# Optimization experiments

Hardware: AMD Instinct MI355X
Metric: run time of the kernel (lower is better)

## Reference

```python
import jax, jax.numpy as jnp
import numpy as np

BATCH = 8192
IN_FEATURES = 1024
OUT_FEATURES = 1024
GRID_SIZE = 5
SPLINE_ORDER = 3
GRID_MIN, GRID_MAX = -1.0, 1.0
NUM_BASES = GRID_SIZE + SPLINE_ORDER  # 8
GRID_LEN = GRID_SIZE + 2 * SPLINE_ORDER + 1  # 12


def setup_inputs() -> dict:
    key = jax.random.key(0)
    k1, k2, k3 = jax.random.split(key, 3)
    x = jax.random.normal(k1, (BATCH, IN_FEATURES), dtype=jnp.float32)
    base_weight = jax.random.normal(k2, (OUT_FEATURES, IN_FEATURES), dtype=jnp.float32) * 0.1
    spline_weight = jax.random.normal(k3, (OUT_FEATURES, IN_FEATURES, NUM_BASES), dtype=jnp.float32) * 0.1
    grid = jnp.linspace(GRID_MIN, GRID_MAX, GRID_LEN, dtype=jnp.float32)  # buffer, not learned
    return {"x": x, "base_weight": base_weight, "spline_weight": spline_weight, "grid": grid}


def _bspline_basis(xc, grid, order):
    """Iterative Cox-de Boor DP, vectorized over all features and basis indices.
    xc: [B, F] clamped inputs; grid: [G] uniform knots (all denominators > 0).
    Returns [B, F, G - order - 1] = [B, F, NUM_BASES]."""
    G = grid.shape[0]
    xe = xc[..., None]  # [B, F, 1]
    # k = 0: indicator of knot interval, matches (x >= grid[i]) & (x < grid[i+1])
    B = ((xe >= grid[:-1]) & (xe < grid[1:])).astype(xc.dtype)  # [B, F, G-1]
    for k in range(1, order + 1):
        left = (xe - grid[: G - k - 1]) / (grid[k : G - 1] - grid[: G - k - 1]) * B[..., :-1]
        right = (grid[k + 1 : G] - xe) / (grid[k + 1 : G] - grid[1 : G - k]) * B[..., 1:]
        B = left + right  # [B, F, G-1-k]
    return B


def reference(x, base_weight, spline_weight, grid):
    # base path: SiLU activation then linear
    base_output = jax.nn.silu(x) @ base_weight.T  # [B, out]
    # spline path: B-spline basis per feature, weighted sum over (in, basis)
    x_clamped = jnp.clip(x, GRID_MIN * 0.99, GRID_MAX * 0.99)
    basis = _bspline_basis(x_clamped, grid, SPLINE_ORDER)  # [B, in, NUM_BASES]
    spline_output = jnp.einsum("bin,oin->bo", basis, spline_weight)
    return base_output + spline_output
```

## Files before the change

### kernel.cpp

```cpp
#include <hip/hip_runtime.h>
#include <stdint.h>

typedef _Float16 f16;
typedef __attribute__((ext_vector_type(8))) _Float16 f16x8;
typedef __attribute__((ext_vector_type(4))) float f32x4;

#define BATCH 8192
#define INF   1024
#define OUTF  1024
#define KTOT  9216
#define NT    72
#define CONV_BLOCKS 4608

__device__ __forceinline__ void gload16(const void* g, void* l) {
  __builtin_amdgcn_global_load_lds(
      (const __attribute__((address_space(1))) uint32_t*)g,
      (__attribute__((address_space(3))) uint32_t*)l, 16, 0, 0);
}

__global__ __launch_bounds__(256) void fused_prep_kernel(
    const float* __restrict__ bw, const float* __restrict__ sw,
    const float* __restrict__ x, const float* __restrict__ grid,
    f16* __restrict__ Wb, f16* __restrict__ Abuf)
{
  int blk = blockIdx.x;
  if (blk < CONV_BLOCKS) {
    int idx = blk * 256 + threadIdx.x;
    int o = idx / 1152;
    int r = idx - o * 1152;
    int k8 = r * 8;
    const float* src = (k8 < INF) ? (bw + (size_t)o * INF + k8)
                                  : (sw + (size_t)o * (INF * 8) + (k8 - INF));
    float4 v0 = *(const float4*)src;
    float4 v1 = *(const float4*)(src + 4);
    f16x8 ov;
    ov[0] = (f16)v0.x; ov[1] = (f16)v0.y; ov[2] = (f16)v0.z; ov[3] = (f16)v0.w;
    ov[4] = (f16)v1.x; ov[5] = (f16)v1.y; ov[6] = (f16)v1.z; ov[7] = (f16)v1.w;
    *(f16x8*)(Wb + (size_t)o * KTOT + k8) = ov;
    return;
  }

  int q = (blk - CONV_BLOCKS) * 256 + threadIdx.x;
  int b = q >> 8;
  int i0 = (q & 255) << 2;
  float4 xv = *(const float4*)(x + ((size_t)b << 10) + i0);
  float xa[4] = {xv.x, xv.y, xv.z, xv.w};

  float g[12];
#pragma unroll
  for (int j = 0; j < 12; ++j) g[j] = grid[j];
  float H  = g[1] - g[0];
  float r1 = 1.0f / H;
  float r2 = 0.5f * r1;
  float r3 = (1.0f / 3.0f) * r1;

  f16 sil[4];
  f16x8 bas[4];
#pragma unroll
  for (int e = 0; e < 4; ++e) {
    float v = xa[e];
    sil[e] = (f16)(v / (1.0f + __expf(-v)));
    float xe = fminf(fmaxf(v, -0.99f), 0.99f);
    float Bv[11];
#pragma unroll
    for (int j = 0; j < 11; ++j) Bv[j] = (xe >= g[j] && xe < g[j + 1]) ? 1.0f : 0.0f;
#pragma unroll
    for (int j = 0; j < 10; ++j) Bv[j] = (xe - g[j]) * r1 * Bv[j] + (g[j + 2] - xe) * r1 * Bv[j + 1];
#pragma unroll
    for (int j = 0; j < 9; ++j)  Bv[j] = (xe - g[j]) * r2 * Bv[j] + (g[j + 3] - xe) * r2 * Bv[j + 1];
#pragma unroll
    for (int j = 0; j < 8; ++j)  Bv[j] = (xe - g[j]) * r3 * Bv[j] + (g[j + 4] - xe) * r3 * Bv[j + 1];
#pragma unroll
    for (int n = 0; n < 8; ++n) bas[e][n] = (f16)Bv[n];
  }
  f16* row = Abuf + (size_t)b * KTOT;
  *(uint64_t*)(row + i0) = *(const uint64_t*)sil;
  f16* bp = row + INF + (size_t)i0 * 8;
#pragma unroll
  for (int e = 0; e < 4; ++e) *(f16x8*)(bp + e * 8) = bas[e];
}

#define LDA(base, m, s) (*(const f16x8*)((base) + ((wr*128 + (m)*16 + la) * 64 + ((((s)*4 + lb) ^ lasw) * 8))))
#define LDB(base, n, s) (*(const f16x8*)((base) + ((wcn*64 + (n)*16 + la) * 64 + ((((s)*4 + lb) ^ lasw) * 8))))

#define MFMA1(m, n, s) acc[m][n] = __builtin_amdgcn_mfma_f32_16x16x32_f16(af[m][s], bf[n][s], acc[m][n], 0, 0, 0)
#define MFMA_S0(m0) do { \
  MFMA1(m0,0,0);   MFMA1(m0,1,0);   MFMA1(m0,2,0);   MFMA1(m0,3,0); \
  MFMA1(m0+1,0,0); MFMA1(m0+1,1,0); MFMA1(m0+1,2,0); MFMA1(m0+1,3,0); } while (0)
#define MFMA_S1(m0) do { \
  MFMA1(m0,0,1);   MFMA1(m0,1,1);   MFMA1(m0,2,1);   MFMA1(m0,3,1); \
  MFMA1(m0+1,0,1); MFMA1(m0+1,1,1); MFMA1(m0+1,2,1); MFMA1(m0+1,3,1); } while (0)

#define SCHED0 __builtin_amdgcn_sched_barrier(0)
#define SBARF do { __builtin_amdgcn_s_barrier(); SCHED0; } while (0)

template <bool ATOMIC>
__global__ __launch_bounds__(512, 2) void kan_gemm_kernel(
    const f16* __restrict__ A, const f16* __restrict__ W,
    float* __restrict__ C, float* __restrict__ P1)
{
  __shared__ __align__(16) f16 lsA[2 * 256 * 64];
  __shared__ __align__(16) f16 lsB[2 * 256 * 64];

  const size_t K = KTOT;
  int bid = blockIdx.x;
  int xcd = bid & 7;
  int u   = bid >> 3;
  int tm  = xcd * 4 + (u & 3);
  int tn  = (u >> 2) & 3;
  int split = u >> 4;
  size_t kbase = (size_t)split * (NT * 64);

  int tid = threadIdx.x;
  int w = tid >> 6, l = tid & 63;
  int wr = w >> 2, wcn = w & 3;
  int la = l & 15, lb = l >> 4, lasw = la & 7;

  int rh = tid >> 3;
  int sc = (tid & 7) ^ (rh & 7);
  const f16* aSrc0 = A + (size_t)(tm * 256 + rh) * K + kbase + sc * 8;
  const f16* bSrc0 = W + (size_t)(tn * 256 + rh) * K + kbase + sc * 8;

  auto stage = [&](int h) {
    if (h >= 4 * NT) return;
    int tile = h >> 2, ty = h & 3, half = ty & 1;
    size_t koff = (size_t)tile * 64;
    if (ty < 2) {
      const f16* s = aSrc0 + (size_t)half * 128 * K + koff;
      f16* d = lsA + (tile & 1) * 16384 + half * 8192 + w * 512;
      gload16(s, d);
      gload16(s + 64 * K, d + 4096);
    } else {
      const f16* s = bSrc0 + (size_t)half * 128 * K + koff;
      f16* d = lsB + (tile & 1) * 16384 + half * 8192 + w * 512;
      gload16(s, d);
      gload16(s + 64 * K, d + 4096);
    }
  };

  f16x8 af[8][2], bf[4][2];
  f32x4 acc[8][4] = {};

  stage(0); stage(1); stage(2); stage(3);
  asm volatile("s_waitcnt vmcnt(0)" ::: "memory");
  SCHED0;

  for (int t = 0; t < NT; ++t) {
    const f16* bA = lsA + (t & 1) * 16384;
    const f16* bB = lsB + (t & 1) * 16384;
    int h1 = 4 * (t + 1);

    SBARF;
    stage(h1 + 0); stage(h1 + 1);
    stage(h1 + 2); stage(h1 + 3);
    __builtin_amdgcn_s_setprio(1);
    af[0][0] = LDA(bA, 0, 0); af[1][0] = LDA(bA, 1, 0);
    bf[0][0] = LDB(bB, 0, 0); bf[1][0] = LDB(bB, 1, 0);
    bf[2][0] = LDB(bB, 2, 0); bf[3][0] = LDB(bB, 3, 0);
    af[0][1] = LDA(bA, 0, 1); af[1][1] = LDA(bA, 1, 1);
    bf[0][1] = LDB(bB, 0, 1); bf[1][1] = LDB(bB, 1, 1);
    bf[2][1] = LDB(bB, 2, 1); bf[3][1] = LDB(bB, 3, 1);
    af[2][0] = LDA(bA, 2, 0); af[3][0] = LDA(bA, 3, 0);
    MFMA_S0(0);
    af[2][1] = LDA(bA, 2, 1); af[3][1] = LDA(bA, 3, 1);
    MFMA_S1(0);
    af[4][0] = LDA(bA, 4, 0); af[5][0] = LDA(bA, 5, 0);
    MFMA_S0(2);
    af[4][1] = LDA(bA, 4, 1); af[5][1] = LDA(bA, 5, 1);
    MFMA_S1(2);
    af[6][0] = LDA(bA, 6, 0); af[7][0] = LDA(bA, 7, 0);
    MFMA_S0(4);
    af[6][1] = LDA(bA, 6, 1); af[7][1] = LDA(bA, 7, 1);
    MFMA_S1(4);
    MFMA_S0(6);
    MFMA_S1(6);
    __builtin_amdgcn_s_setprio(0);
    asm volatile("s_waitcnt vmcnt(0)" ::: "memory");
    SCHED0;
  }

  int rowBase = tm * 256 + wr * 128 + lb * 4;
  int colBase = tn * 256 + wcn * 64 + la;
  float* dst = ATOMIC ? C : (split ? P1 : C);
#pragma unroll
  for (int m = 0; m < 8; ++m)
#pragma unroll
    for (int n = 0; n < 4; ++n) {
      int col = colBase + n * 16;
#pragma unroll
      for (int j = 0; j < 4; ++j) {
        int row = rowBase + m * 16 + j;
        if (ATOMIC) atomicAdd(&C[(size_t)row * OUTF + col], acc[m][n][j]);
        else        dst[(size_t)row * OUTF + col] = acc[m][n][j];
      }
    }
}

__global__ __launch_bounds__(256) void reduce_kernel(
    float* __restrict__ out, const float* __restrict__ p)
{
  size_t i = ((size_t)blockIdx.x * 256 + threadIdx.x) * 4;
  f32x4 a = *(f32x4*)(out + i);
  f32x4 b = *(const f32x4*)(p + i);
  a += b;
  *(f32x4*)(out + i) = a;
}

extern "C" void kernel_launch(void* const* d_in, const int* in_sizes, int n_in,
                              void* d_out, int out_size, void* d_ws, size_t ws_size,
                              hipStream_t stream)
{
  const float* x  = (const float*)d_in[0];
  const float* bw = (const float*)d_in[1];
  const float* sw = (const float*)d_in[2];
  const float* gr = (const float*)d_in[3];
  float* out = (float*)d_out;

  f16* Wb = (f16*)d_ws;
  size_t wBytes = (size_t)OUTF * KTOT * sizeof(f16);
  f16* Abuf = (f16*)((char*)d_ws + wBytes);
  size_t aBytes = (size_t)BATCH * KTOT * sizeof(f16);
  size_t oBytes = (size_t)BATCH * OUTF * sizeof(float);

  int prepBlocks = (BATCH * INF / 4) / 256;
  fused_prep_kernel<<<CONV_BLOCKS + prepBlocks, 256, 0, stream>>>(
      bw, sw, x, gr, Wb, Abuf);

  if (ws_size >= wBytes + aBytes + oBytes) {
    float* P1 = (float*)((char*)d_ws + wBytes + aBytes);
    kan_gemm_kernel<false><<<256, 512, 0, stream>>>(Abuf, Wb, out, P1);
    reduce_kernel<<<(int)(oBytes / sizeof(float) / 4 / 256), 256, 0, stream>>>(out, P1);
  } else {
    hipMemsetAsync(d_out, 0, oBytes, stream);
    kan_gemm_kernel<true><<<256, 512, 0, stream>>>(Abuf, Wb, out, nullptr);
  }
}
```

Measured before the change: 227.9 us.

## Split GEMM main loop into barrier-synchronized load/MFMA phases

Restructures each K-iteration of the fp16 MFMA GEMM into four phases. In each phase the waves load a pair of A fragments from LDS (plus B fragments in the first phase) and issue part of the next tile's global-to-LDS copies. They then meet at a workgroup barrier, wait on lgkmcnt, and run that phase's MFMAs at raised priority. The goal is to keep waves in lockstep, ping-pong style, so LDS reads and MFMA bursts from different waves or blocks interleave better. The cost is many more s_barriers per iteration and full LDS waits before each MFMA group, which can serialize work that was overlapped before.

After: 229.0 us. Within noise of the previous version (+0.5%).

```diff
diff --git a/kernel.cpp b/kernel.cpp
--- a/kernel.cpp
+++ b/kernel.cpp
@@ -92,7 +92,8 @@
   MFMA1(m0+1,0,1); MFMA1(m0+1,1,1); MFMA1(m0+1,2,1); MFMA1(m0+1,3,1); } while (0)
 
 #define SCHED0 __builtin_amdgcn_sched_barrier(0)
-#define SBARF do { __builtin_amdgcn_s_barrier(); SCHED0; } while (0)
+#define SBARF do { SCHED0; __builtin_amdgcn_s_barrier(); SCHED0; } while (0)
+#define LGKM0 do { asm volatile("s_waitcnt lgkmcnt(0)" ::: "memory"); SCHED0; } while (0)
 
 template <bool ATOMIC>
 __global__ __launch_bounds__(512, 2) void kan_gemm_kernel(
@@ -143,40 +144,51 @@
 
   stage(0); stage(1); stage(2); stage(3);
   asm volatile("s_waitcnt vmcnt(0)" ::: "memory");
-  SCHED0;
+  SBARF;
 
   for (int t = 0; t < NT; ++t) {
     const f16* bA = lsA + (t & 1) * 16384;
     const f16* bB = lsB + (t & 1) * 16384;
     int h1 = 4 * (t + 1);
 
-    SBARF;
-    stage(h1 + 0); stage(h1 + 1);
-    stage(h1 + 2); stage(h1 + 3);
-    __builtin_amdgcn_s_setprio(1);
-    af[0][0] = LDA(bA, 0, 0); af[1][0] = LDA(bA, 1, 0);
     bf[0][0] = LDB(bB, 0, 0); bf[1][0] = LDB(bB, 1, 0);
     bf[2][0] = LDB(bB, 2, 0); bf[3][0] = LDB(bB, 3, 0);
-    af[0][1] = LDA(bA, 0, 1); af[1][1] = LDA(bA, 1, 1);
     bf[0][1] = LDB(bB, 0, 1); bf[1][1] = LDB(bB, 1, 1);
     bf[2][1] = LDB(bB, 2, 1); bf[3][1] = LDB(bB, 3, 1);
-    af[2][0] = LDA(bA, 2, 0); af[3][0] = LDA(bA, 3, 0);
-    MFMA_S0(0);
-    af[2][1] = LDA(bA, 2, 1); af[3][1] = LDA(bA, 3, 1);
-    MFMA_S1(0);
-    af[4][0] = LDA(bA, 4, 0); af[5][0] = LDA(bA, 5, 0);
-    MFMA_S0(2);
-    af[4][1] = LDA(bA, 4, 1); af[5][1] = LDA(bA, 5, 1);
-    MFMA_S1(2);
-    af[6][0] = LDA(bA, 6, 0); af[7][0] = LDA(bA, 7, 0);
-    MFMA_S0(4);
-    af[6][1] = LDA(bA, 6, 1); af[7][1] = LDA(bA, 7, 1);
-    MFMA_S1(4);
-    MFMA_S0(6);
-    MFMA_S1(6);
+    af[0][0] = LDA(bA, 0, 0); af[0][1] = LDA(bA, 0, 1);
+    af[1][0] = LDA(bA, 1, 0); af[1][1] = LDA(bA, 1, 1);
+    stage(h1 + 0); stage(h1 + 1);
+    SBARF; LGKM0;
+    __builtin_amdgcn_s_setprio(1);
+    MFMA_S0(0); MFMA_S1(0);
+    __builtin_amdgcn_s_setprio(0);
+    SBARF;
+
+    af[2][0] = LDA(bA, 2, 0); af[2][1] = LDA(bA, 2, 1);
+    af[3][0] = LDA(bA, 3, 0); af[3][1] = LDA(bA, 3, 1);
+    stage(h1 + 2); stage(h1 + 3);
+    SBARF; LGKM0;
+    __builtin_amdgcn_s_setprio(1);
+    MFMA_S0(2); MFMA_S1(2);
+    __builtin_amdgcn_s_setprio(0);
+    SBARF;
+
+    af[4][0] = LDA(bA, 4, 0); af[4][1] = LDA(bA, 4, 1);
+    af[5][0] = LDA(bA, 5, 0); af[5][1] = LDA(bA, 5, 1);
+    SBARF; LGKM0;
+    __builtin_amdgcn_s_setprio(1);
+    MFMA_S0(4); MFMA_S1(4);
+    __builtin_amdgcn_s_setprio(0);
+    SBARF;
+
+    af[6][0] = LDA(bA, 6, 0); af[6][1] = LDA(bA, 6, 1);
+    af[7][0] = LDA(bA, 7, 0); af[7][1] = LDA(bA, 7, 1);
+    SBARF; LGKM0;
+    __builtin_amdgcn_s_setprio(1);
+    MFMA_S0(6); MFMA_S1(6);
     __builtin_amdgcn_s_setprio(0);
     asm volatile("s_waitcnt vmcnt(0)" ::: "memory");
-    SCHED0;
+    SBARF;
   }
 
   int rowBase = tm * 256 + wr * 128 + lb * 4;
```

## Shrink GEMM block to 128x256 tile with single-buffered LDS and mid-loop prefetch

Applied to the files above, without the earlier changes.

Each GEMM block changes from 512 threads with a 256x256 tile and double-buffered LDS to 256 threads with a 128x256 tile and single-buffered LDS. Grid size doubles to 512 blocks. The next tile's global-to-LDS loads are issued halfway through the MFMA work, after all LDS fragments have been read, so they overlap the remaining MFMAs. This lowers LDS use per block so more blocks can be resident, but it reduces reuse of the B tile and adds a second barrier per k-step.

After: 205.6 us. 9.8% less time.

```diff
diff --git a/kernel.cpp b/kernel.cpp
--- a/kernel.cpp
+++ b/kernel.cpp
@@ -80,7 +80,7 @@
   for (int e = 0; e < 4; ++e) *(f16x8*)(bp + e * 8) = bas[e];
 }
 
-#define LDA(base, m, s) (*(const f16x8*)((base) + ((wr*128 + (m)*16 + la) * 64 + ((((s)*4 + lb) ^ lasw) * 8))))
+#define LDA(base, m, s) (*(const f16x8*)((base) + (((m)*16 + la) * 64 + ((((s)*4 + lb) ^ lasw) * 8))))
 #define LDB(base, n, s) (*(const f16x8*)((base) + ((wcn*64 + (n)*16 + la) * 64 + ((((s)*4 + lb) ^ lasw) * 8))))
 
 #define MFMA1(m, n, s) acc[m][n] = __builtin_amdgcn_mfma_f32_16x16x32_f16(af[m][s], bf[n][s], acc[m][n], 0, 0, 0)
@@ -92,94 +92,88 @@
   MFMA1(m0+1,0,1); MFMA1(m0+1,1,1); MFMA1(m0+1,2,1); MFMA1(m0+1,3,1); } while (0)
 
 #define SCHED0 __builtin_amdgcn_sched_barrier(0)
-#define SBARF do { __builtin_amdgcn_s_barrier(); SCHED0; } while (0)
+#define SBARF  do { SCHED0; __builtin_amdgcn_s_barrier(); SCHED0; } while (0)
+#define LGKM0  do { asm volatile("s_waitcnt lgkmcnt(0)" ::: "memory"); SCHED0; } while (0)
 
 template <bool ATOMIC>
-__global__ __launch_bounds__(512, 2) void kan_gemm_kernel(
+__global__ __launch_bounds__(256, 2) void kan_gemm_kernel(
     const f16* __restrict__ A, const f16* __restrict__ W,
     float* __restrict__ C, float* __restrict__ P1)
 {
-  __shared__ __align__(16) f16 lsA[2 * 256 * 64];
-  __shared__ __align__(16) f16 lsB[2 * 256 * 64];
+  __shared__ __align__(16) f16 lsA[128 * 64];
+  __shared__ __align__(16) f16 lsB[256 * 64];
 
   const size_t K = KTOT;
   int bid = blockIdx.x;
   int xcd = bid & 7;
   int u   = bid >> 3;
-  int tm  = xcd * 4 + (u & 3);
-  int tn  = (u >> 2) & 3;
-  int split = u >> 4;
+  int tm  = xcd * 8 + (u & 7);
+  int tn  = (u >> 3) & 3;
+  int split = u >> 5;
   size_t kbase = (size_t)split * (NT * 64);
 
   int tid = threadIdx.x;
   int w = tid >> 6, l = tid & 63;
-  int wr = w >> 2, wcn = w & 3;
+  int wcn = w;
   int la = l & 15, lb = l >> 4, lasw = la & 7;
 
   int rh = tid >> 3;
   int sc = (tid & 7) ^ (rh & 7);
-  const f16* aSrc0 = A + (size_t)(tm * 256 + rh) * K + kbase + sc * 8;
+  const f16* aSrc0 = A + (size_t)(tm * 128 + rh) * K + kbase + sc * 8;
   const f16* bSrc0 = W + (size_t)(tn * 256 + rh) * K + kbase + sc * 8;
 
-  auto stage = [&](int h) {
-    if (h >= 4 * NT) return;
-    int tile = h >> 2, ty = h & 3, half = ty & 1;
-    size_t koff = (size_t)tile * 64;
-    if (ty < 2) {
-      const f16* s = aSrc0 + (size_t)half * 128 * K + koff;
-      f16* d = lsA + (tile & 1) * 16384 + half * 8192 + w * 512;
-      gload16(s, d);
-      gload16(s + 64 * K, d + 4096);
-    } else {
-      const f16* s = bSrc0 + (size_t)half * 128 * K + koff;
-      f16* d = lsB + (tile & 1) * 16384 + half * 8192 + w * 512;
-      gload16(s, d);
-      gload16(s + 64 * K, d + 4096);
-    }
+  auto stageA = [&](int t) {
+    size_t koff = (size_t)t * 64;
+#pragma unroll
+    for (int ln = 0; ln < 4; ++ln)
+      gload16(aSrc0 + (size_t)ln * 32 * K + koff, lsA + ln * 2048 + w * 512);
+  };
+  auto stageB = [&](int t) {
+    size_t koff = (size_t)t * 64;
+#pragma unroll
+    for (int ln = 0; ln < 8; ++ln)
+      gload16(bSrc0 + (size_t)ln * 32 * K + koff, lsB + ln * 2048 + w * 512);
   };
 
   f16x8 af[8][2], bf[4][2];
   f32x4 acc[8][4] = {};
 
-  stage(0); stage(1); stage(2); stage(3);
-  asm volatile("s_waitcnt vmcnt(0)" ::: "memory");
-  SCHED0;
+  stageA(0); stageB(0);
 
   for (int t = 0; t < NT; ++t) {
-    const f16* bA = lsA + (t & 1) * 16384;
-    const f16* bB = lsB + (t & 1) * 16384;
-    int h1 = 4 * (t + 1);
-
+    asm volatile("s_waitcnt vmcnt(0)" ::: "memory");
     SBARF;
-    stage(h1 + 0); stage(h1 + 1);
-    stage(h1 + 2); stage(h1 + 3);
+
+    bf[0][0] = LDB(lsB, 0, 0); bf[1][0] = LDB(lsB, 1, 0);
+    bf[2][0] = LDB(lsB, 2, 0); bf[3][0] = LDB(lsB, 3, 0);
+    bf[0][1] = LDB(lsB, 0, 1); bf[1][1] = LDB(lsB, 1, 1);
+    bf[2][1] = LDB(lsB, 2, 1); bf[3][1] = LDB(lsB, 3, 1);
+    af[0][0] = LDA(lsA, 0, 0); af[0][1] = LDA(lsA, 0, 1);
+    af[1][0] = LDA(lsA, 1, 0); af[1][1] = LDA(lsA, 1, 1);
     __builtin_amdgcn_s_setprio(1);
-    af[0][0] = LDA(bA, 0, 0); af[1][0] = LDA(bA, 1, 0);
-    bf[0][0] = LDB(bB, 0, 0); bf[1][0] = LDB(bB, 1, 0);
-    bf[2][0] = LDB(bB, 2, 0); bf[3][0] = LDB(bB, 3, 0);
-    af[0][1] = LDA(bA, 0, 1); af[1][1] = LDA(bA, 1, 1);
-    bf[0][1] = LDB(bB, 0, 1); bf[1][1] = LDB(bB, 1, 1);
-    bf[2][1] = LDB(bB, 2, 1); bf[3][1] = LDB(bB, 3, 1);
-    af[2][0] = LDA(bA, 2, 0); af[3][0] = LDA(bA, 3, 0);
+    af[2][0] = LDA(lsA, 2, 0); af[3][0] = LDA(lsA, 3, 0);
     MFMA_S0(0);
-    af[2][1] = LDA(bA, 2, 1); af[3][1] = LDA(bA, 3, 1);
+    af[2][1] = LDA(lsA, 2, 1); af[3][1] = LDA(lsA, 3, 1);
     MFMA_S1(0);
-    af[4][0] = LDA(bA, 4, 0); af[5][0] = LDA(bA, 5, 0);
+    af[4][0] = LDA(lsA, 4, 0); af[5][0] = LDA(lsA, 5, 0);
+    af[4][1] = LDA(lsA, 4, 1); af[5][1] = LDA(lsA, 5, 1);
     MFMA_S0(2);
-    af[4][1] = LDA(bA, 4, 1); af[5][1] = LDA(bA, 5, 1);
+    af[6][0] = LDA(lsA, 6, 0); af[7][0] = LDA(lsA, 7, 0);
+    af[6][1] = LDA(lsA, 6, 1); af[7][1] = LDA(lsA, 7, 1);
     MFMA_S1(2);
-    af[6][0] = LDA(bA, 6, 0); af[7][0] = LDA(bA, 7, 0);
-    MFMA_S0(4);
-    af[6][1] = LDA(bA, 6, 1); af[7][1] = LDA(bA, 7, 1);
-    MFMA_S1(4);
-    MFMA_S0(6);
-    MFMA_S1(6);
     __builtin_amdgcn_s_setprio(0);
-    asm volatile("s_waitcnt vmcnt(0)" ::: "memory");
-    SCHED0;
-  }
-
-  int rowBase = tm * 256 + wr * 128 + lb * 4;
+
+    LGKM0;
+    SBARF;
+
+    if (t < NT - 1) { stageA(t + 1); stageB(t + 1); }
+    __builtin_amdgcn_s_setprio(1);
+    MFMA_S0(4); MFMA_S1(4);
+    MFMA_S0(6); MFMA_S1(6);
+    __builtin_amdgcn_s_setprio(0);
+  }
+
+  int rowBase = tm * 128 + lb * 4;
   int colBase = tn * 256 + wcn * 64 + la;
   float* dst = ATOMIC ? C : (split ? P1 : C);
 #pragma unroll
@@ -228,10 +222,10 @@
 
   if (ws_size >= wBytes + aBytes + oBytes) {
     float* P1 = (float*)((char*)d_ws + wBytes + aBytes);
-    kan_gemm_kernel<false><<<256, 512, 0, stream>>>(Abuf, Wb, out, P1);
+    kan_gemm_kernel<false><<<512, 256, 0, stream>>>(Abuf, Wb, out, P1);
     reduce_kernel<<<(int)(oBytes / sizeof(float) / 4 / 256), 256, 0, stream>>>(out, P1);
   } else {
     hipMemsetAsync(d_out, 0, oBytes, stream);
-    kan_gemm_kernel<true><<<256, 512, 0, stream>>>(Abuf, Wb, out, nullptr);
-  }
-}
+    kan_gemm_kernel<true><<<512, 256, 0, stream>>>(Abuf, Wb, out, nullptr);
+  }
+}
```
